# Kernel optimization log

Hardware: AMD Instinct MI355X
Metric: run time of the kernel (lower is better)

## Reference

```python
import jax, jax.numpy as jnp
import numpy as np

# Module hyperparameters (from init_kwargs)
IN_C = 64
OUT_C = 64
K = 3
STRIDE = 1
PAD = 1
DIL = 1
OVERLAP = 4
CENTER_SIZE = 4

# Input sizes
B, H, W = 16, 128, 128


def _crop_mask(h, w):
    """Static (trace-time) crop mask: zeros on the central crop window, ones elsewhere.

    Matches the intended semantics of CropConv's python-loop mask: rows
    [crop_start, crop_start+crop_size) x cols [crop_start, crop_start+crop_size)
    of the HxW output grid are zeroed.
    """
    crop_start = (h - h // CENTER_SIZE) // 2 - OVERLAP  # 44 for h=128
    crop_size = h // CENTER_SIZE + 2 * OVERLAP          # 40 for h=128
    m = np.ones((h, w), dtype=np.float32)
    m[crop_start:crop_start + crop_size, crop_start:crop_start + crop_size] = 0.0
    return jnp.asarray(m)


def setup_inputs() -> dict:
    key = jax.random.key(0)
    kx, kw = jax.random.split(key)
    x = jax.random.normal(kx, (B, IN_C, H, W), dtype=jnp.float32)
    # kaiming_normal_ fan_out init: std = sqrt(2 / (out_channels * k * k))
    w_std = np.sqrt(2.0 / (OUT_C * K * K)).astype(np.float32)
    weight = jax.random.normal(kw, (OUT_C, IN_C, K, K), dtype=jnp.float32) * w_std
    return {"x": x, "weight": weight}


def reference(x, weight):
    # im2col (Unfold) + matmul == a standard dense conv; use the fused conv primitive.
    out = jax.lax.conv_general_dilated(
        x, weight,
        window_strides=(STRIDE, STRIDE),
        padding=((PAD, PAD), (PAD, PAD)),
        rhs_dilation=(DIL, DIL),
        dimension_numbers=("NCHW", "OIHW", "NCHW"),
    )  # [B, OUT_C, H, W] (same-size conv)
    mask = _crop_mask(out.shape[2], out.shape[3])  # [H, W], {0,1}
    # torch.where(mask, out, 0) == out * mask (mask is constant wrt grads)
    return out * mask
```

## Files before the change

kernel.cpp:

```cpp
#include <hip/hip_runtime.h>
#include <stdint.h>


#define B_ 16
#define C_ 64
#define H_ 128
#define W_ 128

#define TCOLS_A 130
#define XLDS_A (3 * TCOLS_A * 8)

typedef float f32x4 __attribute__((ext_vector_type(4)));
typedef short bf16x8 __attribute__((ext_vector_type(8)));

__device__ inline unsigned short f2bf(float f) {
    union { float f; uint32_t u; } v; v.f = f;
    uint32_t u = v.u + 0x7FFF + ((v.u >> 16) & 1);
    return (unsigned short)(u >> 16);
}

__global__ __launch_bounds__(256) void xform_weight(
    const float* __restrict__ wgt, uint16_t* __restrict__ Wb)
{
    int L = blockIdx.x * 256 + threadIdx.x;
    int e    = L & 7;
    int lane = (L >> 3) & 63;
    int i    = (L >> 9) & 3;
    int ch   = (L >> 11) & 1;
    int kk   = L >> 12;
    int oc   = i * 16 + (lane & 15);
    int ic   = ch * 32 + (lane >> 4) * 8 + e;
    Wb[L] = f2bf(wgt[((size_t)oc * 64 + ic) * 9 + kk]);
}

__global__ __launch_bounds__(256, 3) void conv_main(
    const uint4* __restrict__ Wq,
    const float* __restrict__ x,
    float* __restrict__ out)
{
    __shared__ uint4 lds[XLDS_A];

    const int t    = threadIdx.x;
    const int lane = t & 63;
    const int wv   = t >> 6;
    const int n    = lane & 15;
    const int q    = lane >> 4;

    const int d    = blockIdx.x;
    const int orig = (d & 7) * 256 + (d >> 3);
    const int ht   = orig & 127;
    const int b    = orig >> 7;

    {
        const int c4    = t & 31;
        const int j     = t >> 5;
        const int cbase = 1 + c4 * 4;
        const int wg0   = c4 * 4;

        #pragma unroll
        for (int r = 0; r < 3; ++r) {
            const int h = ht - 1 + r;
            if (h < 0 || h >= H_) {
                uint4 z; z.x = z.y = z.z = z.w = 0;
                #pragma unroll
                for (int cc = 0; cc < 4; ++cc)
                    lds[(r * TCOLS_A + cbase + cc) * 8 +
                        ((j + cbase + cc) & 7)] = z;
            } else {
                const float* src =
                    x + (((size_t)(b * C_ + j * 8)) * H_ + h) * W_ + wg0;
                f32x4 f[8];
                #pragma unroll
                for (int e = 0; e < 8; ++e)
                    f[e] = *(const f32x4*)(src + (size_t)e * (H_ * W_));
                #pragma unroll
                for (int cc = 0; cc < 4; ++cc) {
                    uint32_t u[4];
                    #pragma unroll
                    for (int p = 0; p < 4; ++p)
                        u[p] = (uint32_t)f2bf(f[2 * p][cc]) |
                               ((uint32_t)f2bf(f[2 * p + 1][cc]) << 16);
                    lds[(r * TCOLS_A + cbase + cc) * 8 +
                        ((j + cbase + cc) & 7)] = *(const uint4*)u;
                }
            }
        }
        if (t < 48) {
            const int ce = (t < 24) ? 0 : (TCOLS_A - 1);
            const int u  = (t < 24) ? t : t - 24;
            const int r  = u >> 3, jj = u & 7;
            uint4 z; z.x = z.y = z.z = z.w = 0;
            lds[(r * TCOLS_A + ce) * 8 + ((jj + ce) & 7)] = z;
        }
    }
    __syncthreads();

    f32x4 acc[2][4];
    #pragma unroll
    for (int i = 0; i < 2; ++i)
        #pragma unroll
        for (int f = 0; f < 4; ++f)
            acc[i][f] = (f32x4){0.f, 0.f, 0.f, 0.f};

    const int ohalf = wv & 1;
    const int wq    = (wv >> 1) * 64;

    #pragma unroll
    for (int kh = 0; kh < 3; ++kh) {
        #pragma unroll
        for (int kw = 0; kw < 3; ++kw) {
            const int kk = kh * 3 + kw;
            #pragma unroll
            for (int ch = 0; ch < 2; ++ch) {
                bf16x8 a[2], bb[4];
                #pragma unroll
                for (int i = 0; i < 2; ++i)
                    a[i] = __builtin_bit_cast(bf16x8,
                        Wq[((kk * 2 + ch) * 4 + ohalf * 2 + i) * 64 + lane]);
                #pragma unroll
                for (int f = 0; f < 4; ++f) {
                    const int ct  = wq + f * 16 + n + kw;
                    const int idx = (kh * TCOLS_A + ct) * 8 +
                                    ((ch * 4 + q + ct) & 7);
                    bb[f] = __builtin_bit_cast(bf16x8, lds[idx]);
                }
                #pragma unroll
                for (int i = 0; i < 2; ++i)
                    #pragma unroll
                    for (int f = 0; f < 4; ++f)
                        acc[i][f] = __builtin_amdgcn_mfma_f32_16x16x32_bf16(
                            a[i], bb[f], acc[i][f], 0, 0, 0);
            }
        }
    }

    const int  h  = ht;
    const bool hz = (h >= 44 && h < 84);
    #pragma unroll
    for (int f = 0; f < 4; ++f) {
        const int w0 = wq + f * 16 + n;
        const bool zz = hz && (w0 >= 44 && w0 < 84);
        #pragma unroll
        for (int i = 0; i < 2; ++i) {
            #pragma unroll
            for (int r = 0; r < 4; ++r) {
                const int oc = ohalf * 32 + i * 16 + q * 4 + r;
                out[(((size_t)b * C_ + oc) * H_ + h) * W_ + w0] =
                    zz ? 0.f : acc[i][f][r];
            }
        }
    }
}

#define WLDS_U4 4608
#define FXLDS_U4 4096

__global__ __launch_bounds__(256, 1) void conv_fused(
    const float* __restrict__ x,
    const float* __restrict__ wgt,
    float* __restrict__ out)
{
    __shared__ uint4 lds[WLDS_U4 + FXLDS_U4];
    uint16_t* lds16 = (uint16_t*)lds;

    const int t    = threadIdx.x;
    const int lane = t & 63;
    const int wv   = t >> 6;
    const int n    = lane & 15;
    const int q    = lane >> 4;

    const int d    = blockIdx.x;
    const int orig = (d & 7) * 128 + (d >> 3);
    const int b    = orig >> 6;
    const int h0   = (orig & 63) * 2;

    #pragma unroll
    for (int p = 0; p < 2; ++p) {
        const int a_  = t + 256 * p;
        const int oc  = a_ >> 3;
        const int oct = a_ & 7;
        const float* src = wgt + (size_t)oc * 576 + (size_t)oct * 72;
        f32x4 w4[18];
        #pragma unroll
        for (int j = 0; j < 18; ++j) w4[j] = ((const f32x4*)src)[j];
        const int ch = oct >> 2, qq = oct & 3;
        const int ii = oc >> 4,  nn = oc & 15;
        #pragma unroll
        for (int kk = 0; kk < 9; ++kk) {
            #define WELEM(e) ((uint32_t)f2bf(w4[((e)*9 + kk) >> 2][((e)*9 + kk) & 3]))
            uint4 val;
            val.x = WELEM(0) | (WELEM(1) << 16);
            val.y = WELEM(2) | (WELEM(3) << 16);
            val.z = WELEM(4) | (WELEM(5) << 16);
            val.w = WELEM(6) | (WELEM(7) << 16);
            #undef WELEM
            lds[((kk * 2 + ch) * 4 + ii) * 64 + qq * 16 + nn] = val;
        }
    }

    {
        const int ic    = t >> 2;
        const int w0    = (t & 3) * 32;
        const int jslot = ic >> 3;
        const int esub  = ic & 7;
        #pragma unroll
        for (int r = 0; r < 4; ++r) {
            const int h = h0 - 1 + r;
            if (h < 0 || h >= H_) {
                uint4 z; z.x = z.y = z.z = z.w = 0;
                #pragma unroll
                for (int k = 0; k < 4; ++k)
                    lds[WLDS_U4 + r * 1024 + k * 256 + t] = z;
            } else {
                const float* src =
                    x + (((size_t)(b * C_ + ic)) * H_ + h) * W_ + w0;
                f32x4 v4[8];
                #pragma unroll
                for (int j = 0; j < 8; ++j) v4[j] = ((const f32x4*)src)[j];
                #pragma unroll
                for (int k = 0; k < 32; ++k) {
                    const int c    = w0 + k;
                    const int slot = (jslot + c) & 7;
                    lds16[WLDS_U4 * 8 + ((r * 128 + c) * 8 + slot) * 8 + esub] =
                        f2bf(v4[k >> 2][k & 3]);
                }
            }
        }
    }
    __syncthreads();

    f32x4 acc[4][4];
    #pragma unroll
    for (int i = 0; i < 4; ++i)
        #pragma unroll
        for (int tt = 0; tt < 4; ++tt)
            acc[i][tt] = (f32x4){0.f, 0.f, 0.f, 0.f};

    const int wb = (wv & 1) * 64;
    const uint4* Wl = lds;
    const uint4* Xl = lds + WLDS_U4;
    const bool lz = (wb + n) == 0;
    const bool rz = (wb + n) == 79;
    const bf16x8 zfrag = 0;

    #pragma unroll
    for (int kh = 0; kh < 3; ++kh) {
        const int row = (wv >> 1) + kh;
        #pragma unroll
        for (int kw = 0; kw < 3; ++kw) {
            const int kk = kh * 3 + kw;
            #pragma unroll
            for (int ch = 0; ch < 2; ++ch) {
                bf16x8 a[4], bb[4];
                #pragma unroll
                for (int i = 0; i < 4; ++i)
                    a[i] = __builtin_bit_cast(bf16x8,
                        Wl[((kk * 2 + ch) * 4 + i) * 64 + lane]);
                #pragma unroll
                for (int tt = 0; tt < 4; ++tt) {
                    int c   = wb + tt * 16 + n + kw - 1;
                    int cc  = min(max(c, 0), 127);
                    int idx = (row * 128 + cc) * 8 + ((ch * 4 + q + cc) & 7);
                    bf16x8 v = __builtin_bit_cast(bf16x8, Xl[idx]);
                    if (kw == 0 && tt == 0) v = lz ? zfrag : v;
                    if (kw == 2 && tt == 3) v = rz ? zfrag : v;
                    bb[tt] = v;
                }
                #pragma unroll
                for (int i = 0; i < 4; ++i)
                    #pragma unroll
                    for (int tt = 0; tt < 4; ++tt)
                        acc[i][tt] = __builtin_amdgcn_mfma_f32_16x16x32_bf16(
                            a[i], bb[tt], acc[i][tt], 0, 0, 0);
            }
        }
    }

    const int  h  = h0 + (wv >> 1);
    const bool hz = (h >= 44 && h < 84);
    #pragma unroll
    for (int i = 0; i < 4; ++i) {
        #pragma unroll
        for (int tt = 0; tt < 4; ++tt) {
            const int  w0 = wb + tt * 16 + n;
            const bool zz = hz && (w0 >= 44 && w0 < 84);
            #pragma unroll
            for (int r = 0; r < 4; ++r) {
                const int oc = i * 16 + q * 4 + r;
                out[(((size_t)b * C_ + oc) * H_ + h) * W_ + w0] =
                    zz ? 0.f : acc[i][tt][r];
            }
        }
    }
}

extern "C" void kernel_launch(void* const* d_in, const int* in_sizes, int n_in,
                              void* d_out, int out_size, void* d_ws, size_t ws_size,
                              hipStream_t stream) {
    const float* x   = (const float*)d_in[0];
    const float* wgt = (const float*)d_in[1];
    float* out       = (float*)d_out;

    const size_t W_BYTES = 9 * 2 * 4 * 64 * 16;
    if (ws_size >= W_BYTES) {
        uint16_t* Wb = (uint16_t*)d_ws;
        xform_weight<<<dim3(144), dim3(256), 0, stream>>>(wgt, Wb);
        conv_main<<<dim3(2048), dim3(256), 0, stream>>>(
            (const uint4*)Wb, x, out);
    } else {
        conv_fused<<<dim3(1024), dim3(256), 0, stream>>>(x, wgt, out);
    }
}
```

Before: 135.8 us.

## Stage input channels in two halves to shrink LDS and raise occupancy

The conv_main kernel now stages the 3-row input tile in two 32-channel halves, reusing a smaller LDS buffer with a barrier between halves. The buffer uses a padded row stride (131 columns per channel group) in place of the XOR swizzle, and launch bounds go from 3 to 5 blocks per CU. The aim is more resident blocks to hide global-load latency. In exchange, each block pays an extra synchronization and a second serialized load phase, and the padded layout may give different LDS bank-conflict behaviour.

Result: slower. 154.4 us (+13.7%).

```diff
diff --git a/kernel.cpp b/kernel.cpp
--- a/kernel.cpp
+++ b/kernel.cpp
@@ -7,8 +7,9 @@
 #define H_ 128
 #define W_ 128
 
-#define TCOLS_A 130
-#define XLDS_A (3 * TCOLS_A * 8)
+#define TCOLS_B 131
+#define ROWSTRIDE (4 * TCOLS_B)
+#define XLDS_B (3 * ROWSTRIDE)
 
 typedef float f32x4 __attribute__((ext_vector_type(4)));
 typedef short bf16x8 __attribute__((ext_vector_type(8)));
@@ -33,12 +34,42 @@
     Wb[L] = f2bf(wgt[((size_t)oc * 64 + ic) * 9 + kk]);
 }
 
-__global__ __launch_bounds__(256, 3) void conv_main(
+__device__ __forceinline__ void stage_task(
+    uint4* lds, const float* __restrict__ xb, int ht,
+    int r, int j, int c4, int ch)
+{
+    const int cbase = 1 + c4 * 4;
+    const int h     = ht - 1 + r;
+    uint4* dst = lds + r * ROWSTRIDE + j * TCOLS_B + cbase;
+    if (h < 0 || h >= H_) {
+        uint4 z; z.x = z.y = z.z = z.w = 0;
+        #pragma unroll
+        for (int cc = 0; cc < 4; ++cc) dst[cc] = z;
+    } else {
+        const float* src =
+            xb + ((size_t)(ch * 32 + j * 8) * H_ + h) * W_ + c4 * 4;
+        f32x4 f[8];
+        #pragma unroll
+        for (int e = 0; e < 8; ++e)
+            f[e] = *(const f32x4*)(src + (size_t)e * (H_ * W_));
+        #pragma unroll
+        for (int cc = 0; cc < 4; ++cc) {
+            uint32_t u[4];
+            #pragma unroll
+            for (int p = 0; p < 4; ++p)
+                u[p] = (uint32_t)f2bf(f[2 * p][cc]) |
+                       ((uint32_t)f2bf(f[2 * p + 1][cc]) << 16);
+            dst[cc] = *(const uint4*)u;
+        }
+    }
+}
+
+__global__ __launch_bounds__(256, 5) void conv_main(
     const uint4* __restrict__ Wq,
     const float* __restrict__ x,
     float* __restrict__ out)
 {
-    __shared__ uint4 lds[XLDS_A];
+    __shared__ uint4 lds[XLDS_B];
 
     const int t    = threadIdx.x;
     const int lane = t & 63;
@@ -51,49 +82,14 @@
     const int ht   = orig & 127;
     const int b    = orig >> 7;
 
-    {
-        const int c4    = t & 31;
-        const int j     = t >> 5;
-        const int cbase = 1 + c4 * 4;
-        const int wg0   = c4 * 4;
-
-        #pragma unroll
-        for (int r = 0; r < 3; ++r) {
-            const int h = ht - 1 + r;
-            if (h < 0 || h >= H_) {
-                uint4 z; z.x = z.y = z.z = z.w = 0;
-                #pragma unroll
-                for (int cc = 0; cc < 4; ++cc)
-                    lds[(r * TCOLS_A + cbase + cc) * 8 +
-                        ((j + cbase + cc) & 7)] = z;
-            } else {
-                const float* src =
-                    x + (((size_t)(b * C_ + j * 8)) * H_ + h) * W_ + wg0;
-                f32x4 f[8];
-                #pragma unroll
-                for (int e = 0; e < 8; ++e)
-                    f[e] = *(const f32x4*)(src + (size_t)e * (H_ * W_));
-                #pragma unroll
-                for (int cc = 0; cc < 4; ++cc) {
-                    uint32_t u[4];
-                    #pragma unroll
-                    for (int p = 0; p < 4; ++p)
-                        u[p] = (uint32_t)f2bf(f[2 * p][cc]) |
-                               ((uint32_t)f2bf(f[2 * p + 1][cc]) << 16);
-                    lds[(r * TCOLS_A + cbase + cc) * 8 +
-                        ((j + cbase + cc) & 7)] = *(const uint4*)u;
-                }
-            }
-        }
-        if (t < 48) {
-            const int ce = (t < 24) ? 0 : (TCOLS_A - 1);
-            const int u  = (t < 24) ? t : t - 24;
-            const int r  = u >> 3, jj = u & 7;
-            uint4 z; z.x = z.y = z.z = z.w = 0;
-            lds[(r * TCOLS_A + ce) * 8 + ((jj + ce) & 7)] = z;
-        }
-    }
-    __syncthreads();
+    const int ohalf = wv & 1;
+    const int wq    = (wv >> 1) * 64;
+
+    const float* xb = x + (size_t)b * C_ * H_ * W_;
+
+    const int r1  = t >> 7;
+    const int c41 = (t & 127) >> 2;
+    const int j1  = t & 3;
 
     f32x4 acc[2][4];
     #pragma unroll
@@ -102,16 +98,26 @@
         for (int f = 0; f < 4; ++f)
             acc[i][f] = (f32x4){0.f, 0.f, 0.f, 0.f};
 
-    const int ohalf = wv & 1;
-    const int wq    = (wv >> 1) * 64;
-
-    #pragma unroll
-    for (int kh = 0; kh < 3; ++kh) {
-        #pragma unroll
-        for (int kw = 0; kw < 3; ++kw) {
-            const int kk = kh * 3 + kw;
-            #pragma unroll
-            for (int ch = 0; ch < 2; ++ch) {
+    #pragma unroll
+    for (int ch = 0; ch < 2; ++ch) {
+        if (ch) __syncthreads();
+
+        stage_task(lds, xb, ht, r1, j1, c41, ch);
+        if (t < 128) stage_task(lds, xb, ht, 2, j1, c41, ch);
+        if (t < 24) {
+            const int ce = (t < 12) ? 0 : 129;
+            const int u  = (t < 12) ? t : t - 12;
+            const int r  = u >> 2, jj = u & 3;
+            uint4 z; z.x = z.y = z.z = z.w = 0;
+            lds[r * ROWSTRIDE + jj * TCOLS_B + ce] = z;
+        }
+        __syncthreads();
+
+        #pragma unroll
+        for (int kh = 0; kh < 3; ++kh) {
+            #pragma unroll
+            for (int kw = 0; kw < 3; ++kw) {
+                const int kk = kh * 3 + kw;
                 bf16x8 a[2], bb[4];
                 #pragma unroll
                 for (int i = 0; i < 2; ++i)
@@ -119,10 +125,9 @@
                         Wq[((kk * 2 + ch) * 4 + ohalf * 2 + i) * 64 + lane]);
                 #pragma unroll
                 for (int f = 0; f < 4; ++f) {
-                    const int ct  = wq + f * 16 + n + kw;
-                    const int idx = (kh * TCOLS_A + ct) * 8 +
-                                    ((ch * 4 + q + ct) & 7);
-                    bb[f] = __builtin_bit_cast(bf16x8, lds[idx]);
+                    const int ct = wq + f * 16 + n + kw;
+                    bb[f] = __builtin_bit_cast(bf16x8,
+                        lds[kh * ROWSTRIDE + q * TCOLS_B + ct]);
                 }
                 #pragma unroll
                 for (int i = 0; i < 2; ++i)
@@ -134,8 +139,7 @@
         }
     }
 
-    const int  h  = ht;
-    const bool hz = (h >= 44 && h < 84);
+    const bool hz = (ht >= 44 && ht < 84);
     #pragma unroll
     for (int f = 0; f < 4; ++f) {
         const int w0 = wq + f * 16 + n;
@@ -145,7 +149,7 @@
             #pragma unroll
             for (int r = 0; r < 4; ++r) {
                 const int oc = ohalf * 32 + i * 16 + q * 4 + r;
-                out[(((size_t)b * C_ + oc) * H_ + h) * W_ + w0] =
+                out[(((size_t)b * C_ + oc) * H_ + ht) * W_ + w0] =
                     zz ? 0.f : acc[i][f][r];
             }
         }
```

## Compute two output rows per block to reuse staged input halo rows

Applied to the files above, without the earlier changes.

Each block now handles two adjacent output rows with 512 threads instead of one row with 256. It stages four input rows into LDS rather than three per output row, which cuts redundant global loads and bf16 conversion of the vertical halo from 3x to 2x. Waves are split across row, output-channel half and width half. The trade-off is a larger LDS footprint per block and fewer blocks in the grid, which can change occupancy.

After: 145.6 us. 7.2% more time.

```diff
diff --git a/kernel.cpp b/kernel.cpp
--- a/kernel.cpp
+++ b/kernel.cpp
@@ -8,7 +8,8 @@
 #define W_ 128
 
 #define TCOLS_A 130
-#define XLDS_A (3 * TCOLS_A * 8)
+#define ROWU4   (TCOLS_A * 8)
+#define XLDS_C  (4 * ROWU4)
 
 typedef float f32x4 __attribute__((ext_vector_type(4)));
 typedef short bf16x8 __attribute__((ext_vector_type(8)));
@@ -33,12 +34,12 @@
     Wb[L] = f2bf(wgt[((size_t)oc * 64 + ic) * 9 + kk]);
 }
 
-__global__ __launch_bounds__(256, 3) void conv_main(
+__global__ __launch_bounds__(512, 4) void conv_main(
     const uint4* __restrict__ Wq,
     const float* __restrict__ x,
     float* __restrict__ out)
 {
-    __shared__ uint4 lds[XLDS_A];
+    __shared__ uint4 lds[XLDS_C];
 
     const int t    = threadIdx.x;
     const int lane = t & 63;
@@ -47,28 +48,37 @@
     const int q    = lane >> 4;
 
     const int d    = blockIdx.x;
-    const int orig = (d & 7) * 256 + (d >> 3);
-    const int ht   = orig & 127;
-    const int b    = orig >> 7;
+    const int orig = (d & 7) * 128 + (d >> 3);
+    const int hp   = orig & 63;
+    const int b    = orig >> 6;
+    const int h0   = hp * 2;
+
+    const int hh    = wv & 1;
+    const int ohalf = (wv >> 1) & 1;
+    const int whalf = wv >> 2;
+    const int wqb   = whalf * 64;
+
+    const float* xb = x + (size_t)b * C_ * H_ * W_;
 
     {
-        const int c4    = t & 31;
-        const int j     = t >> 5;
+        const int j     = t & 7;
+        const int c4    = (t >> 3) & 31;
+        const int rr    = t >> 8;
         const int cbase = 1 + c4 * 4;
         const int wg0   = c4 * 4;
 
         #pragma unroll
-        for (int r = 0; r < 3; ++r) {
-            const int h = ht - 1 + r;
+        for (int p = 0; p < 2; ++p) {
+            const int r = rr + p * 2;
+            const int h = h0 - 1 + r;
             if (h < 0 || h >= H_) {
                 uint4 z; z.x = z.y = z.z = z.w = 0;
                 #pragma unroll
                 for (int cc = 0; cc < 4; ++cc)
-                    lds[(r * TCOLS_A + cbase + cc) * 8 +
+                    lds[r * ROWU4 + (cbase + cc) * 8 +
                         ((j + cbase + cc) & 7)] = z;
             } else {
-                const float* src =
-                    x + (((size_t)(b * C_ + j * 8)) * H_ + h) * W_ + wg0;
+                const float* src = xb + ((size_t)(j * 8) * H_ + h) * W_ + wg0;
                 f32x4 f[8];
                 #pragma unroll
                 for (int e = 0; e < 8; ++e)
@@ -77,20 +87,20 @@
                 for (int cc = 0; cc < 4; ++cc) {
                     uint32_t u[4];
                     #pragma unroll
-                    for (int p = 0; p < 4; ++p)
-                        u[p] = (uint32_t)f2bf(f[2 * p][cc]) |
-                               ((uint32_t)f2bf(f[2 * p + 1][cc]) << 16);
-                    lds[(r * TCOLS_A + cbase + cc) * 8 +
+                    for (int pp = 0; pp < 4; ++pp)
+                        u[pp] = (uint32_t)f2bf(f[2 * pp][cc]) |
+                                ((uint32_t)f2bf(f[2 * pp + 1][cc]) << 16);
+                    lds[r * ROWU4 + (cbase + cc) * 8 +
                         ((j + cbase + cc) & 7)] = *(const uint4*)u;
                 }
             }
         }
-        if (t < 48) {
-            const int ce = (t < 24) ? 0 : (TCOLS_A - 1);
-            const int u  = (t < 24) ? t : t - 24;
+        if (t < 64) {
+            const int ce = (t < 32) ? 0 : (TCOLS_A - 1);
+            const int u  = t & 31;
             const int r  = u >> 3, jj = u & 7;
             uint4 z; z.x = z.y = z.z = z.w = 0;
-            lds[(r * TCOLS_A + ce) * 8 + ((jj + ce) & 7)] = z;
+            lds[r * ROWU4 + ce * 8 + ((jj + ce) & 7)] = z;
         }
     }
     __syncthreads();
@@ -101,9 +111,6 @@
         #pragma unroll
         for (int f = 0; f < 4; ++f)
             acc[i][f] = (f32x4){0.f, 0.f, 0.f, 0.f};
-
-    const int ohalf = wv & 1;
-    const int wq    = (wv >> 1) * 64;
 
     #pragma unroll
     for (int kh = 0; kh < 3; ++kh) {
@@ -119,8 +126,9 @@
                         Wq[((kk * 2 + ch) * 4 + ohalf * 2 + i) * 64 + lane]);
                 #pragma unroll
                 for (int f = 0; f < 4; ++f) {
-                    const int ct  = wq + f * 16 + n + kw;
-                    const int idx = (kh * TCOLS_A + ct) * 8 +
+                    const int row = hh + kh;
+                    const int ct  = wqb + f * 16 + n + kw;
+                    const int idx = row * ROWU4 + ct * 8 +
                                     ((ch * 4 + q + ct) & 7);
                     bb[f] = __builtin_bit_cast(bf16x8, lds[idx]);
                 }
@@ -134,11 +142,11 @@
         }
     }
 
-    const int  h  = ht;
+    const int  h  = h0 + hh;
     const bool hz = (h >= 44 && h < 84);
     #pragma unroll
     for (int f = 0; f < 4; ++f) {
-        const int w0 = wq + f * 16 + n;
+        const int w0 = wqb + f * 16 + n;
         const bool zz = hz && (w0 >= 44 && w0 < 84);
         #pragma unroll
         for (int i = 0; i < 2; ++i) {
@@ -305,7 +313,7 @@
     if (ws_size >= W_BYTES) {
         uint16_t* Wb = (uint16_t*)d_ws;
         xform_weight<<<dim3(144), dim3(256), 0, stream>>>(wgt, Wb);
-        conv_main<<<dim3(2048), dim3(256), 0, stream>>>(
+        conv_main<<<dim3(1024), dim3(512), 0, stream>>>(
             (const uint4*)Wb, x, out);
     } else {
         conv_fused<<<dim3(1024), dim3(256), 0, stream>>>(x, wgt, out);
```
